# Kernel optimization log

Measured on AMD Instinct MI355X. Metric: run time of the kernel, lower is better.

Reference implementation:

```python
import jax, jax.numpy as jnp
import numpy as np


def setup_inputs() -> dict:
    key = jax.random.key(0)
    ks = jax.random.split(key, 8)
    B, N, C = 8, 4096, 128
    x = jax.random.normal(ks[0], (B, N, C), dtype=jnp.float32)
    spatial_pos = jax.random.randint(ks[1], (1, N, N), 0, 6, dtype=jnp.int32)
    sc = 1.0 / np.sqrt(C)
    W1 = jax.random.normal(ks[2], (C, C), dtype=jnp.float32) * sc
    b1 = jax.random.normal(ks[3], (C,), dtype=jnp.float32) * 0.01
    W2 = jax.random.normal(ks[4], (C, C // 8), dtype=jnp.float32) * sc
    b2 = jax.random.normal(ks[5], (C // 8,), dtype=jnp.float32) * 0.01
    Wb = jax.random.normal(ks[6], (C + C // 8, C), dtype=jnp.float32) * (1.0 / np.sqrt(C + C // 8))
    bb = jax.random.normal(ks[7], (C,), dtype=jnp.float32) * 0.01
    return {"x": x, "spatial_pos": spatial_pos, "W1": W1, "b1": b1,
            "W2": W2, "b2": b2, "Wb": Wb, "bb": bb}


def reference(x, spatial_pos, W1, b1, W2, b2, Wb, bb):
    # s=1, l=2: scale k=1 uses mask (spatial_pos <= 1), k=2 uses (spatial_pos == 2)
    sp = spatial_pos[0]                      # [N, N], batch-invariant
    m1 = (sp <= 1).astype(x.dtype)           # [N, N]
    m2 = (sp == 2).astype(x.dtype)           # [N, N]
    h1 = x @ W1 + b1                         # [B, N, C]
    h2 = x @ W2 + b2                         # [B, N, C//8]
    # torch.bmm(mask.expand(B,-1,-1), h) == einsum over shared mask
    f1 = jnp.einsum('ij,bjc->bic', m1, h1)   # [B, N, C]
    f2 = jnp.einsum('ij,bjc->bic', m2, h2)   # [B, N, C//8]
    feats = jnp.concatenate([f1, f2], axis=-1)  # [B, N, C + C//8]
    return feats @ Wb + bb                   # [B, N, output_dim]
```

## Files before the change

### kernel.cpp

```cpp
#include <hip/hip_runtime.h>
#include <stdint.h>

typedef unsigned short u16;
typedef __attribute__((ext_vector_type(8))) short short8;
typedef __attribute__((ext_vector_type(4))) float f32x4;

#define MFMA __builtin_amdgcn_mfma_f32_16x16x32_bf16

__device__ __forceinline__ u16 f2bf(float f) {
  union { float f; uint32_t u; } v; v.f = f;
  return (u16)((v.u + 0x7FFFu + ((v.u >> 16) & 1u)) >> 16);
}

#define GLOAD16(gp, lp) \
  __builtin_amdgcn_global_load_lds((const __attribute__((address_space(1))) uint32_t*)(gp), \
                                   (__attribute__((address_space(3))) uint32_t*)(lp), 16, 0, 0)

#define WS_H    0
#define WS_Q1   9502720
#define WS_Q2   9503232
#define WS_M1P  9503744
#define WS_M2P  11600896
#define WS_RS1  13698048
#define WS_RS2  13714432
#define WS_WSB  13730816

__global__ __launch_bounds__(256) void k0(const int* __restrict__ sp,
                                          unsigned long long* __restrict__ m1p,
                                          unsigned long long* __restrict__ m2p,
                                          float* __restrict__ rs1, float* __restrict__ rs2,
                                          const float* __restrict__ W1, const float* __restrict__ Wb,
                                          const float* __restrict__ b1, const float* __restrict__ b2,
                                          const float* __restrict__ W2,
                                          float* __restrict__ q1, float* __restrict__ q2,
                                          u16* __restrict__ wsbg) {
  const int tid = threadIdx.x;
  if (blockIdx.x < 1024) {
    int wave = tid >> 6, lane = tid & 63;
    int i = blockIdx.x * 4 + wave;
    const int* rowp = sp + (size_t)i * 4096;
    int c1 = 0, c2 = 0;
    for (int w = 0; w < 64; ++w) {
      int v = rowp[w * 64 + lane];
      unsigned long long bb1 = __ballot(v <= 1);
      unsigned long long bb2 = __ballot(v == 2);
      if (lane == 0) {
        m1p[(size_t)w * 4096 + i] = bb1;
        m2p[(size_t)w * 4096 + i] = bb2;
        c1 += __popcll(bb1);
        c2 += __popcll(bb2);
      }
    }
    if (lane == 0) { rs1[i] = (float)c1; rs2[i] = (float)c2; }
    return;
  }
  int idx = (int)(blockIdx.x - 1024) * 256 + tid;
  int a = idx >> 7, c = idx & 127;
  float acc = 0.f;
  for (int k = 0; k < 128; ++k) acc += W1[a * 128 + k] * Wb[k * 128 + c];
  wsbg[(((a >> 3) * 144) + c) * 8 + (a & 7)] = f2bf(acc);
  if (idx < 2048) {
    int k = idx >> 4, nn2 = idx & 15;
    wsbg[(((k >> 3) * 144) + 128 + nn2) * 8 + (k & 7)] = f2bf(W2[k * 16 + nn2]);
  }
  if (idx < 128) {
    float s1 = 0.f, s2 = 0.f;
    for (int k = 0; k < 128; ++k) s1 += b1[k] * Wb[k * 128 + idx];
    for (int k = 0; k < 16; ++k)  s2 += b2[k] * Wb[(128 + k) * 128 + idx];
    q1[idx] = s1; q2[idx] = s2;
  }
}

__global__ __launch_bounds__(512, 1) void kproj(const float* __restrict__ x,
                                                const u16* __restrict__ wsbg,
                                                u16* __restrict__ H) {
  __shared__ u16 wsb[18432];
  __shared__ u16 xs[128 * 136];
  __shared__ u16 hs[128 * 146];
  const int tid = threadIdx.x;
  const int bid = blockIdx.x;
  const int r0 = bid * 128;
  const int b = bid >> 5;
  const int kt0 = (bid & 31) * 2;

  {
    const int e0 = tid * 8;
    GLOAD16(wsbg + e0,         (char*)&wsb[0] + e0 * 2);
    GLOAD16(wsbg + 4096 + e0,  (char*)&wsb[0] + (4096 + e0) * 2);
    GLOAD16(wsbg + 8192 + e0,  (char*)&wsb[0] + (8192 + e0) * 2);
    GLOAD16(wsbg + 12288 + e0, (char*)&wsb[0] + (12288 + e0) * 2);
    if (tid < 256)
      GLOAD16(wsbg + 16384 + e0, (char*)&wsb[0] + (16384 + e0) * 2);
  }
  {
    const float* xp = x + ((size_t)(r0 + (tid >> 2))) * 128 + (tid & 3) * 32;
    u16* xd = xs + (tid >> 2) * 136 + (tid & 3) * 32;
#pragma unroll
    for (int i = 0; i < 4; ++i) {
      f32x4 a = ((const f32x4*)xp)[i * 2];
      f32x4 bq = ((const f32x4*)xp)[i * 2 + 1];
      short8 pk;
      pk[0] = (short)f2bf(a[0]); pk[1] = (short)f2bf(a[1]);
      pk[2] = (short)f2bf(a[2]); pk[3] = (short)f2bf(a[3]);
      pk[4] = (short)f2bf(bq[0]); pk[5] = (short)f2bf(bq[1]);
      pk[6] = (short)f2bf(bq[2]); pk[7] = (short)f2bf(bq[3]);
      *(short8*)(xd + i * 8) = pk;
    }
  }
  __syncthreads();

  const int w = tid >> 6, l = tid & 63, lr = l & 15, lg = l >> 4;
  f32x4 acc[9];
  f32x4 zz = {0.f, 0.f, 0.f, 0.f};
#pragma unroll
  for (int fn = 0; fn < 9; ++fn) acc[fn] = zz;
#pragma unroll
  for (int kf = 0; kf < 4; ++kf) {
    short8 af = *(const short8*)(xs + (w * 16 + lr) * 136 + kf * 32 + lg * 8);
#pragma unroll
    for (int fn = 0; fn < 9; ++fn) {
      short8 bf = *(const short8*)(wsb + (((kf * 4 + lg) * 144) + fn * 16 + lr) * 8);
      acc[fn] = MFMA(af, bf, acc[fn], 0, 0, 0);
    }
  }
  __syncthreads();
#pragma unroll
  for (int fn = 0; fn < 9; ++fn)
#pragma unroll
    for (int g = 0; g < 4; ++g)
      hs[(w * 16 + lg * 4 + g) * 146 + fn * 16 + lr] = f2bf(acc[fn][g]);
  __syncthreads();
  for (int i = 0; i < 5; ++i) {
    int e = i * 512 + tid;
    if (e < 2304) {
      int slab = e / 1152, rem = e % 1152;
      int jbl = rem / 144, n = rem % 144;
      union { u16 s[8]; uint4 v; } pk;
#pragma unroll
      for (int r = 0; r < 8; ++r) pk.s[r] = hs[(slab * 64 + jbl * 8 + r) * 146 + n];
      int kf = jbl >> 2, lgw = jbl & 3, fn = n >> 4, lrw = n & 15;
      size_t di = ((((size_t)(kt0 + slab) * 2 + kf) * 8 + b) * 9 + fn) * 512 + (lgw * 16 + lrw) * 8;
      *(uint4*)(H + di) = pk.v;
    }
  }
}

__device__ __forceinline__ short8 expand_byte(uint32_t wd, int lgsh) {
  uint32_t b = (wd >> lgsh) & 0xFFu;
  uint32_t t = b * 0x8001u;
  union { uint32_t u[4]; short8 s; } r;
  r.u[0] = (t & 0x00010001u) * 0x3F80u;
  r.u[1] = (t & 0x00040004u) * 0x0FE0u;
  r.u[2] = (t & 0x00100010u) * 0x03F8u;
  r.u[3] = (t & 0x00400040u) * 0x00FEu;
  return r.s;
}

__global__ __launch_bounds__(1024, 4) void kb1(const u16* __restrict__ H,
                                               const char* __restrict__ M1b,
                                               const char* __restrict__ M2b,
                                               const float* __restrict__ rs1, const float* __restrict__ rs2,
                                               const float* __restrict__ q1, const float* __restrict__ q2,
                                               const float* __restrict__ Wb, const float* __restrict__ bb,
                                               float* __restrict__ out) {
  __shared__ u16 bt[3][9216];
  __shared__ u16 mkb[3][1024];
  __shared__ float f2pf[2][128][16];
  __shared__ u16 f2s[128 * 40];
  __shared__ u16 wb2s[4096];

  const int tid = threadIdx.x;
  const int bid = blockIdx.x;
  const int b = bid & 7;
  const int i0 = (bid >> 3) * 128;

  const int w = tid >> 6, l = tid & 63, lr = l & 15, lg = l >> 4;
  const int g = w >> 2, c = w & 3;
  const int fm2 = w & 7, kf2 = w >> 3;
  const int lgsh = lg * 8;

  const uint32_t cA = tid, cB = 1024 + tid;
  const uint32_t offA = (cA < 576) ? (b * 4608 + cA * 8) : (36864 + b * 4608 + (cA - 576) * 8);
  const uint32_t offB = 36864 + b * 4608 + (cB - 576) * 8;
  const u16* pB1 = H + offA;
  const u16* pB2 = H + offB;
  const char* pM = (((tid & 64) ? M2b : M1b)) + (size_t)i0 * 8 + (size_t)(tid & 63) * 16;
  const int d1 = tid * 16;
  const int d2 = 16384 + tid * 16;
  const int dM = (tid - 128) * 16;

#define STAGE(BUF) { \
    GLOAD16(pB1, (char*)&bt[BUF][0] + d1); \
    if (tid < 128) GLOAD16(pB2, (char*)&bt[BUF][0] + d2); \
    else if (tid < 256) GLOAD16(pM, (char*)&mkb[BUF][0] + dM); \
    pB1 += 73728; pB2 += 73728; pM += 32768; }

  const int fA0 = (c * 2 + 0) * 512 + l * 8;
  const int fA1 = (c * 2 + 1) * 512 + l * 8;
  const int fB0 = 4608 + fA0;
  const int fB1 = 4608 + fA1;
  const int fM  = kf2 * 4608 + 4096 + l * 8;

  f32x4 zz = {0.f, 0.f, 0.f, 0.f};
  f32x4 acc00 = zz, acc01 = zz, acc10 = zz, acc11 = zz;
  f32x4 acc2 = zz;

#define WAITV { if (w < 4) asm volatile("s_waitcnt vmcnt(2)" ::: "memory"); \
                else asm volatile("s_waitcnt vmcnt(1)" ::: "memory"); }

#define COMPUTE(BUF) { \
    const u16* src_ = &bt[BUF][0]; \
    const char* mk_ = (const char*)&mkb[BUF][0]; \
    uint2 c0_ = *(const uint2*)(mk_ + ((g * 2 + 0) * 16 + lr) * 8); \
    uint2 c1_ = *(const uint2*)(mk_ + ((g * 2 + 1) * 16 + lr) * 8); \
    uint32_t c2_ = *(const uint32_t*)(mk_ + 1024 + (fm2 * 16 + lr) * 8 + kf2 * 4); \
    short8 bA0_ = *(const short8*)(src_ + fA0); \
    short8 bA1_ = *(const short8*)(src_ + fA1); \
    short8 bB0_ = *(const short8*)(src_ + fB0); \
    short8 bB1_ = *(const short8*)(src_ + fB1); \
    short8 bM_  = *(const short8*)(src_ + fM); \
    short8 e0x_ = expand_byte(c0_.x, lgsh), e0y_ = expand_byte(c0_.y, lgsh); \
    short8 e1x_ = expand_byte(c1_.x, lgsh), e1y_ = expand_byte(c1_.y, lgsh); \
    short8 e2v_ = expand_byte(c2_, lgsh); \
    __builtin_amdgcn_s_setprio(1); \
    acc00 = MFMA(e0x_, bA0_, acc00, 0, 0, 0); \
    acc01 = MFMA(e0x_, bA1_, acc01, 0, 0, 0); \
    acc00 = MFMA(e0y_, bB0_, acc00, 0, 0, 0); \
    acc01 = MFMA(e0y_, bB1_, acc01, 0, 0, 0); \
    acc10 = MFMA(e1x_, bA0_, acc10, 0, 0, 0); \
    acc11 = MFMA(e1x_, bA1_, acc11, 0, 0, 0); \
    acc10 = MFMA(e1y_, bB0_, acc10, 0, 0, 0); \
    acc11 = MFMA(e1y_, bB1_, acc11, 0, 0, 0); \
    acc2  = MFMA(e2v_, bM_, acc2, 0, 0, 0); \
    __builtin_amdgcn_s_setprio(0); }

#define PHASE(BUF, BUF2) { WAITV; __builtin_amdgcn_s_barrier(); STAGE(BUF2); COMPUTE(BUF) }

  STAGE(0);
  STAGE(1);

#pragma unroll
  for (int i = 0; i < 4; ++i) {
    int e = i * 1024 + tid;
    int r_ = e & 7, nn = (e >> 3) & 127, jb = e >> 10;
    int k = jb * 8 + r_;
    wb2s[e] = f2bf((k < 16) ? Wb[(128 + k) * 128 + nn] : 0.f);
  }

  for (int it = 0; it < 20; ++it) {
    PHASE(0, 2);
    PHASE(1, 0);
    PHASE(2, 1);
  }
  PHASE(0, 2);
  PHASE(1, 0);
  { WAITV; __builtin_amdgcn_s_barrier(); COMPUTE(2) }
  { asm volatile("s_waitcnt vmcnt(0)" ::: "memory");
    __builtin_amdgcn_s_barrier(); COMPUTE(0) }

#pragma unroll
  for (int gg = 0; gg < 4; ++gg)
    f2pf[kf2][fm2 * 16 + lg * 4 + gg][lr] = acc2[gg];
  __syncthreads();
#pragma unroll
  for (int j = 0; j < 2; ++j) {
    int e = j * 1024 + tid;
    int row = e >> 4, col = e & 15;
    f2s[row * 40 + col] = f2bf(f2pf[0][row][col] + f2pf[1][row][col]);
    f2s[row * 40 + 16 + col] = 0;
  }
  __syncthreads();

  short8 bw0 = *(const short8*)(wb2s + ((lg * 128) + (c * 2 + 0) * 16 + lr) * 8);
  short8 bw1 = *(const short8*)(wb2s + ((lg * 128) + (c * 2 + 1) * 16 + lr) * 8);
  {
    short8 af0 = *(const short8*)(f2s + ((g * 2 + 0) * 16 + lr) * 40 + lg * 8);
    short8 af1 = *(const short8*)(f2s + ((g * 2 + 1) * 16 + lr) * 40 + lg * 8);
    acc00 = MFMA(af0, bw0, acc00, 0, 0, 0);
    acc01 = MFMA(af0, bw1, acc01, 0, 0, 0);
    acc10 = MFMA(af1, bw0, acc10, 0, 0, 0);
    acc11 = MFMA(af1, bw1, acc11, 0, 0, 0);
  }

  const int col0 = (c * 2 + 0) * 16 + lr, col1 = (c * 2 + 1) * 16 + lr;
  const float q10 = q1[col0], q20 = q2[col0], bb0 = bb[col0];
  const float q11 = q1[col1], q21 = q2[col1], bb1 = bb[col1];
#pragma unroll
  for (int i = 0; i < 2; ++i) {
    f32x4 a0 = i ? acc10 : acc00;
    f32x4 a1 = i ? acc11 : acc01;
#pragma unroll
    for (int gg = 0; gg < 4; ++gg) {
      int row = (g * 2 + i) * 16 + lg * 4 + gg;
      float r1 = rs1[i0 + row], r2 = rs2[i0 + row];
      size_t obase = ((size_t)b * 4096 + i0 + row) * 128;
      out[obase + col0] = a0[gg] + r1 * q10 + r2 * q20 + bb0;
      out[obase + col1] = a1[gg] + r1 * q11 + r2 * q21 + bb1;
    }
  }
}

extern "C" void kernel_launch(void* const* d_in, const int* in_sizes, int n_in,
                              void* d_out, int out_size, void* d_ws, size_t ws_size,
                              hipStream_t stream) {
  const float* x  = (const float*)d_in[0];
  const int*   sp = (const int*)d_in[1];
  const float* W1 = (const float*)d_in[2];
  const float* b1 = (const float*)d_in[3];
  const float* W2 = (const float*)d_in[4];
  const float* b2 = (const float*)d_in[5];
  const float* Wb = (const float*)d_in[6];
  const float* bb = (const float*)d_in[7];
  float* out = (float*)d_out;
  char* ws = (char*)d_ws;

  u16* H = (u16*)(ws + WS_H);
  float* q1 = (float*)(ws + WS_Q1);
  float* q2 = (float*)(ws + WS_Q2);
  unsigned long long* m1p = (unsigned long long*)(ws + WS_M1P);
  unsigned long long* m2p = (unsigned long long*)(ws + WS_M2P);
  float* rs1 = (float*)(ws + WS_RS1);
  float* rs2 = (float*)(ws + WS_RS2);
  u16* wsbg = (u16*)(ws + WS_WSB);

  k0<<<1088, 256, 0, stream>>>(sp, m1p, m2p, rs1, rs2, W1, Wb, b1, b2, W2, q1, q2, wsbg);
  kproj<<<256, 512, 0, stream>>>(x, wsbg, H);
  kb1<<<256, 1024, 0, stream>>>(H, (const char*)m1p, (const char*)m2p,
                                rs1, rs2, q1, q2, Wb, bb, out);
}
```

Before: 92.82 us.

## Double K-slab staging in kb1, load masks into registers, split kproj blocks

The main kb1 loop now stages two K-slabs of H per pipeline stage into larger LDS buffers. That halves the number of barrier phases. Mask bits are loaded straight from global memory into registers, prefetched one stage ahead, so they no longer go through LDS. kproj is split into 512 blocks of 256 threads, each handling 64 rows, which allows two blocks per CU. The cost is more LDS per kb1 block, more registers for the prefetched masks, and uncoalesced small global loads for the mask words.

```diff
diff --git a/kernel.cpp b/kernel.cpp
--- a/kernel.cpp
+++ b/kernel.cpp
@@ -71,29 +71,23 @@
   }
 }
 
-__global__ __launch_bounds__(512, 1) void kproj(const float* __restrict__ x,
+__global__ __launch_bounds__(256, 2) void kproj(const float* __restrict__ x,
                                                 const u16* __restrict__ wsbg,
                                                 u16* __restrict__ H) {
   __shared__ u16 wsb[18432];
-  __shared__ u16 xs[128 * 136];
-  __shared__ u16 hs[128 * 146];
+  __shared__ u16 xs[64 * 136];
+  __shared__ u16 hs[64 * 146];
   const int tid = threadIdx.x;
   const int bid = blockIdx.x;
-  const int r0 = bid * 128;
-  const int b = bid >> 5;
-  const int kt0 = (bid & 31) * 2;
-
+  const int b = bid >> 6;
+  const int kt = bid & 63;
+  const size_t r0 = (size_t)b * 4096 + (size_t)kt * 64;
+
+#pragma unroll
+  for (int i = 0; i < 9; ++i)
+    GLOAD16(wsbg + (i * 256 + tid) * 8, (char*)&wsb[0] + (i * 256 + tid) * 16);
   {
-    const int e0 = tid * 8;
-    GLOAD16(wsbg + e0,         (char*)&wsb[0] + e0 * 2);
-    GLOAD16(wsbg + 4096 + e0,  (char*)&wsb[0] + (4096 + e0) * 2);
-    GLOAD16(wsbg + 8192 + e0,  (char*)&wsb[0] + (8192 + e0) * 2);
-    GLOAD16(wsbg + 12288 + e0, (char*)&wsb[0] + (12288 + e0) * 2);
-    if (tid < 256)
-      GLOAD16(wsbg + 16384 + e0, (char*)&wsb[0] + (16384 + e0) * 2);
-  }
-  {
-    const float* xp = x + ((size_t)(r0 + (tid >> 2))) * 128 + (tid & 3) * 32;
+    const float* xp = x + (r0 + (tid >> 2)) * 128 + (tid & 3) * 32;
     u16* xd = xs + (tid >> 2) * 136 + (tid & 3) * 32;
 #pragma unroll
     for (int i = 0; i < 4; ++i) {
@@ -131,15 +125,14 @@
       hs[(w * 16 + lg * 4 + g) * 146 + fn * 16 + lr] = f2bf(acc[fn][g]);
   __syncthreads();
   for (int i = 0; i < 5; ++i) {
-    int e = i * 512 + tid;
-    if (e < 2304) {
-      int slab = e / 1152, rem = e % 1152;
-      int jbl = rem / 144, n = rem % 144;
+    int e = i * 256 + tid;
+    if (e < 1152) {
+      int jbl = e / 144, n = e % 144;
       union { u16 s[8]; uint4 v; } pk;
 #pragma unroll
-      for (int r = 0; r < 8; ++r) pk.s[r] = hs[(slab * 64 + jbl * 8 + r) * 146 + n];
+      for (int r = 0; r < 8; ++r) pk.s[r] = hs[(jbl * 8 + r) * 146 + n];
       int kf = jbl >> 2, lgw = jbl & 3, fn = n >> 4, lrw = n & 15;
-      size_t di = ((((size_t)(kt0 + slab) * 2 + kf) * 8 + b) * 9 + fn) * 512 + (lgw * 16 + lrw) * 8;
+      size_t di = ((((size_t)kt * 2 + kf) * 8 + b) * 9 + fn) * 512 + (lgw * 16 + lrw) * 8;
       *(uint4*)(H + di) = pk.v;
     }
   }
@@ -157,14 +150,13 @@
 }
 
 __global__ __launch_bounds__(1024, 4) void kb1(const u16* __restrict__ H,
-                                               const char* __restrict__ M1b,
-                                               const char* __restrict__ M2b,
+                                               const uint2* __restrict__ M1,
+                                               const uint32_t* __restrict__ M2w,
                                                const float* __restrict__ rs1, const float* __restrict__ rs2,
                                                const float* __restrict__ q1, const float* __restrict__ q2,
                                                const float* __restrict__ Wb, const float* __restrict__ bb,
                                                float* __restrict__ out) {
-  __shared__ u16 bt[3][9216];
-  __shared__ u16 mkb[3][1024];
+  __shared__ u16 bt[3][18432];
   __shared__ float f2pf[2][128][16];
   __shared__ u16 f2s[128 * 40];
   __shared__ u16 wb2s[4096];
@@ -179,21 +171,42 @@
   const int fm2 = w & 7, kf2 = w >> 3;
   const int lgsh = lg * 8;
 
-  const uint32_t cA = tid, cB = 1024 + tid;
-  const uint32_t offA = (cA < 576) ? (b * 4608 + cA * 8) : (36864 + b * 4608 + (cA - 576) * 8);
-  const uint32_t offB = 36864 + b * 4608 + (cB - 576) * 8;
-  const u16* pB1 = H + offA;
-  const u16* pB2 = H + offB;
-  const char* pM = (((tid & 64) ? M2b : M1b)) + (size_t)i0 * 8 + (size_t)(tid & 63) * 16;
-  const int d1 = tid * 16;
-  const int d2 = 16384 + tid * 16;
-  const int dM = (tid - 128) * 16;
+#pragma unroll
+  for (int i = 0; i < 4; ++i) {
+    int e = i * 1024 + tid;
+    int r_ = e & 7, nn = (e >> 3) & 127, jb = e >> 10;
+    int k = jb * 8 + r_;
+    wb2s[e] = f2bf((k < 16) ? Wb[(128 + k) * 128 + nn] : 0.f);
+  }
+
+  auto choff = [&](int ch) -> uint32_t {
+    int slab = (ch >= 1152) ? 1 : 0;
+    int r = ch - slab * 1152;
+    return (uint32_t)(slab * 73728 + (r < 576 ? b * 4608 + r * 8 : 36864 + b * 4608 + (r - 576) * 8));
+  };
+  const u16* pB0 = H + choff(tid);
+  const u16* pB1 = H + choff(1024 + tid);
+  const u16* pB2 = H + choff(tid < 256 ? 2048 + tid : 2048);
+  const int dB0 = tid * 16, dB1 = (1024 + tid) * 16, dB2 = (2048 + tid) * 16;
 
 #define STAGE(BUF) { \
-    GLOAD16(pB1, (char*)&bt[BUF][0] + d1); \
-    if (tid < 128) GLOAD16(pB2, (char*)&bt[BUF][0] + d2); \
-    else if (tid < 256) GLOAD16(pM, (char*)&mkb[BUF][0] + dM); \
-    pB1 += 73728; pB2 += 73728; pM += 32768; }
+    GLOAD16(pB0, (char*)&bt[BUF][0] + dB0); \
+    GLOAD16(pB1, (char*)&bt[BUF][0] + dB1); \
+    if (tid < 256) GLOAD16(pB2, (char*)&bt[BUF][0] + dB2); \
+    pB0 += 147456; pB1 += 147456; pB2 += 147456; }
+
+  const uint2* mp1a = M1 + i0 + (g * 2 + 0) * 16 + lr;
+  const uint2* mp1b = M1 + i0 + (g * 2 + 1) * 16 + lr;
+  const uint32_t* mp2 = M2w + (size_t)(i0 + fm2 * 16 + lr) * 2 + kf2;
+  size_t mo1 = 0, mo2 = 0;
+
+  uint2 PA0, PB0, PA1, PB1, QA0, QB0, QA1, QB1, RA0, RB0, RA1, RB1;
+  uint32_t PC0, PC1, QC0, QC1, RC0, RC1;
+
+#define MLOAD(S) { \
+    S##A0 = mp1a[mo1]; S##B0 = mp1b[mo1]; S##C0 = mp2[mo2]; \
+    S##A1 = mp1a[mo1 + 4096]; S##B1 = mp1b[mo1 + 4096]; S##C1 = mp2[mo2 + 8192]; \
+    mo1 += 8192; mo2 += 16384; }
 
   const int fA0 = (c * 2 + 0) * 512 + l * 8;
   const int fA1 = (c * 2 + 1) * 512 + l * 8;
@@ -205,23 +218,19 @@
   f32x4 acc00 = zz, acc01 = zz, acc10 = zz, acc11 = zz;
   f32x4 acc2 = zz;
 
-#define WAITV { if (w < 4) asm volatile("s_waitcnt vmcnt(2)" ::: "memory"); \
-                else asm volatile("s_waitcnt vmcnt(1)" ::: "memory"); }
-
-#define COMPUTE(BUF) { \
-    const u16* src_ = &bt[BUF][0]; \
-    const char* mk_ = (const char*)&mkb[BUF][0]; \
-    uint2 c0_ = *(const uint2*)(mk_ + ((g * 2 + 0) * 16 + lr) * 8); \
-    uint2 c1_ = *(const uint2*)(mk_ + ((g * 2 + 1) * 16 + lr) * 8); \
-    uint32_t c2_ = *(const uint32_t*)(mk_ + 1024 + (fm2 * 16 + lr) * 8 + kf2 * 4); \
+#define WAITV { if (w < 4) asm volatile("s_waitcnt vmcnt(3)" ::: "memory"); \
+                else asm volatile("s_waitcnt vmcnt(2)" ::: "memory"); }
+
+#define CKT(BUF, S, MA, MB, MC) { \
+    const u16* src_ = &bt[BUF][(S) * 9216]; \
     short8 bA0_ = *(const short8*)(src_ + fA0); \
     short8 bA1_ = *(const short8*)(src_ + fA1); \
     short8 bB0_ = *(const short8*)(src_ + fB0); \
     short8 bB1_ = *(const short8*)(src_ + fB1); \
     short8 bM_  = *(const short8*)(src_ + fM); \
-    short8 e0x_ = expand_byte(c0_.x, lgsh), e0y_ = expand_byte(c0_.y, lgsh); \
-    short8 e1x_ = expand_byte(c1_.x, lgsh), e1y_ = expand_byte(c1_.y, lgsh); \
-    short8 e2v_ = expand_byte(c2_, lgsh); \
+    short8 e0x_ = expand_byte(MA.x, lgsh), e0y_ = expand_byte(MA.y, lgsh); \
+    short8 e1x_ = expand_byte(MB.x, lgsh), e1y_ = expand_byte(MB.y, lgsh); \
+    short8 e2v_ = expand_byte(MC, lgsh); \
     __builtin_amdgcn_s_setprio(1); \
     acc00 = MFMA(e0x_, bA0_, acc00, 0, 0, 0); \
     acc01 = MFMA(e0x_, bA1_, acc01, 0, 0, 0); \
@@ -234,29 +243,20 @@
     acc2  = MFMA(e2v_, bM_, acc2, 0, 0, 0); \
     __builtin_amdgcn_s_setprio(0); }
 
-#define PHASE(BUF, BUF2) { WAITV; __builtin_amdgcn_s_barrier(); STAGE(BUF2); COMPUTE(BUF) }
-
+#define COMPUTE2(BUF, S) { CKT(BUF, 0, S##A0, S##B0, S##C0) CKT(BUF, 1, S##A1, S##B1, S##C1) }
+
+  MLOAD(P);
   STAGE(0);
   STAGE(1);
 
-#pragma unroll
-  for (int i = 0; i < 4; ++i) {
-    int e = i * 1024 + tid;
-    int r_ = e & 7, nn = (e >> 3) & 127, jb = e >> 10;
-    int k = jb * 8 + r_;
-    wb2s[e] = f2bf((k < 16) ? Wb[(128 + k) * 128 + nn] : 0.f);
-  }
-
-  for (int it = 0; it < 20; ++it) {
-    PHASE(0, 2);
-    PHASE(1, 0);
-    PHASE(2, 1);
-  }
-  PHASE(0, 2);
-  PHASE(1, 0);
-  { WAITV; __builtin_amdgcn_s_barrier(); COMPUTE(2) }
-  { asm volatile("s_waitcnt vmcnt(0)" ::: "memory");
-    __builtin_amdgcn_s_barrier(); COMPUTE(0) }
+  for (int it = 0; it < 10; ++it) {
+    WAITV; __builtin_amdgcn_s_barrier(); MLOAD(Q); STAGE(2); COMPUTE2(0, P);
+    WAITV; __builtin_amdgcn_s_barrier(); MLOAD(R); STAGE(0); COMPUTE2(1, Q);
+    WAITV; __builtin_amdgcn_s_barrier(); MLOAD(P); STAGE(1); COMPUTE2(2, R);
+  }
+  WAITV; __builtin_amdgcn_s_barrier(); MLOAD(Q); COMPUTE2(0, P);
+  asm volatile("s_waitcnt vmcnt(0)" ::: "memory");
+  __builtin_amdgcn_s_barrier(); COMPUTE2(1, Q);
 
 #pragma unroll
   for (int gg = 0; gg < 4; ++gg)
@@ -324,7 +324,7 @@
   u16* wsbg = (u16*)(ws + WS_WSB);
 
   k0<<<1088, 256, 0, stream>>>(sp, m1p, m2p, rs1, rs2, W1, Wb, b1, b2, W2, q1, q2, wsbg);
-  kproj<<<256, 512, 0, stream>>>(x, wsbg, H);
-  kb1<<<256, 1024, 0, stream>>>(H, (const char*)m1p, (const char*)m2p,
+  kproj<<<512, 256, 0, stream>>>(x, wsbg, H);
+  kb1<<<256, 1024, 0, stream>>>(H, (const uint2*)m1p, (const uint32_t*)m2p,
                                 rs1, rs2, q1, q2, Wb, bb, out);
 }
```

After: 101.1 us. 8.9% more time.
